# Kernel tuning notes

Hardware: AMD Instinct MI355X
Metric: run time of the kernel (lower is better)

## Reference

```python
import jax, jax.numpy as jnp
import numpy as np

CHANNELS = 256
NUM_HEADS = 4
NUM_GROUPS = 8
EPS = 1e-5


def setup_inputs() -> dict:
    key = jax.random.key(0)
    ks = jax.random.split(key, 7)
    c = CHANNELS
    x = jax.random.normal(ks[0], (2, c, 16, 16, 16), dtype=jnp.float32)
    # GroupNorm affine params (torch init: weight=1, bias=0)
    norm_w = jnp.ones((c,), dtype=jnp.float32)
    norm_b = jnp.zeros((c,), dtype=jnp.float32)
    # 1x1x1 Conv3d weights stored as [out_ch, in_ch]
    fan = 1.0 / np.sqrt(c)
    qkv_w = jax.random.uniform(ks[1], (3 * c, c), minval=-fan, maxval=fan, dtype=jnp.float32)
    qkv_b = jax.random.uniform(ks[2], (3 * c,), minval=-fan, maxval=fan, dtype=jnp.float32)
    proj_w = jax.random.uniform(ks[3], (c, c), minval=-fan, maxval=fan, dtype=jnp.float32)
    proj_b = jax.random.uniform(ks[4], (c,), minval=-fan, maxval=fan, dtype=jnp.float32)
    return {"x": x, "norm_w": norm_w, "norm_b": norm_b,
            "qkv_w": qkv_w, "qkv_b": qkv_b, "proj_w": proj_w, "proj_b": proj_b}


def _group_norm(x, w, b):
    B, C, D, H, W = x.shape
    g = NUM_GROUPS
    xg = x.reshape(B, g, C // g, D, H, W)
    mean = xg.mean(axis=(2, 3, 4, 5), keepdims=True)
    var = xg.var(axis=(2, 3, 4, 5), keepdims=True)
    xg = (xg - mean) * jax.lax.rsqrt(var + EPS)
    x = xg.reshape(B, C, D, H, W)
    return x * w[None, :, None, None, None] + b[None, :, None, None, None]


def _conv1x1(x, w, b):
    # x: [B, Cin, D, H, W], w: [Cout, Cin]
    y = jnp.einsum('bcdhw,oc->bodhw', x, w)
    return y + b[None, :, None, None, None]


def reference(x, norm_w, norm_b, qkv_w, qkv_b, proj_w, proj_b):
    B, C, D, H, W = x.shape
    N = D * H * W
    hd = C // NUM_HEADS
    x_norm = _group_norm(x, norm_w, norm_b)
    qkv = _conv1x1(x_norm, qkv_w, qkv_b)  # [B, 3C, D, H, W]
    q, k, v = jnp.split(qkv, 3, axis=1)
    q = q.reshape(B, NUM_HEADS, hd, N)
    k = k.reshape(B, NUM_HEADS, hd, N)
    v = v.reshape(B, NUM_HEADS, hd, N)
    scale = hd ** -0.5
    # attn[b,h,n,m] = softmax_m(q[:, :, :, n] . k[:, :, :, m] * scale)
    scores = jnp.einsum('bhcn,bhcm->bhnm', q, k) * scale
    attn = jax.nn.softmax(scores, axis=-1)
    out = jnp.einsum('bhcm,bhnm->bhcn', v, attn)
    out = out.reshape(B, C, D, H, W)
    return _conv1x1(out, proj_w, proj_b) + x
```

## Files before the change

kernel.cpp:

```cpp
#include <hip/hip_runtime.h>
#include <hip/hip_bf16.h>

#define NSP 4096
#define CH 256
#define NB 2
#define NG 8
#define CPG 32
#define NHD 4
#define HDIM 64

typedef unsigned short u16;
typedef unsigned int u32;
typedef __attribute__((ext_vector_type(8))) short bf16x8;
typedef __attribute__((ext_vector_type(4))) float f32x4;

#define MFMA __builtin_amdgcn_mfma_f32_16x16x32_bf16
#define QSCALE 0.18033688f

__device__ __forceinline__ u16 f2bf(float f) {
    u32 i = __float_as_uint(f);
    u32 r = (i + 0x7FFFu + ((i >> 16) & 1u)) >> 16;
    return (u16)r;
}

__device__ __forceinline__ void dma16(const u16* g, u16* l) {
    __builtin_amdgcn_global_load_lds(
        (const __attribute__((address_space(1))) void*)g,
        (__attribute__((address_space(3))) void*)l, 16, 0, 0);
}

__global__ __launch_bounds__(256) void prep(const float* __restrict__ qw,
                                            const float* __restrict__ pw,
                                            u16* __restrict__ wqb,
                                            u16* __restrict__ wpb,
                                            const float* __restrict__ x,
                                            float* __restrict__ partial) {
    if (blockIdx.x < 256) {
        int i = (blockIdx.x * 256 + threadIdx.x) * 4;
        const float* src; u16* dstbase; int j;
        if (i < 3 * CH * CH) { src = qw + i; dstbase = wqb; j = i; }
        else { j = i - 3 * CH * CH; src = pw + j; dstbase = wpb; }
        int m = j >> 8, c = j & 255;
        int dc = ((((c >> 3) ^ (m & 7)) << 3)) | (c & 7);
        float4 v = *(const float4*)src;
        ushort4 o;
        o.x = f2bf(v.x); o.y = f2bf(v.y); o.z = f2bf(v.z); o.w = f2bf(v.w);
        *(ushort4*)(dstbase + (m << 8) + dc) = o;
        return;
    }
    const int id = blockIdx.x - 256;
    const int bg = id >> 4, chunk = id & 15;
    const float* p = x + (size_t)bg * (CPG * NSP) + chunk * 8192;
    float s = 0.f, ss = 0.f;
    for (int i = threadIdx.x; i < 2048; i += 256) {
        float4 u = ((const float4*)p)[i];
        s += u.x + u.y + u.z + u.w;
        ss += u.x * u.x + u.y * u.y + u.z * u.z + u.w * u.w;
    }
    for (int off = 32; off > 0; off >>= 1) {
        s += __shfl_down(s, off);
        ss += __shfl_down(ss, off);
    }
    __shared__ float red[4][2];
    const int wv = threadIdx.x >> 6;
    if ((threadIdx.x & 63) == 0) { red[wv][0] = s; red[wv][1] = ss; }
    __syncthreads();
    if (threadIdx.x == 0) {
        float ts = red[0][0] + red[1][0] + red[2][0] + red[3][0];
        float tq = red[0][1] + red[1][1] + red[2][1] + red[3][1];
        partial[(bg * 16 + chunk) * 2]     = ts;
        partial[(bg * 16 + chunk) * 2 + 1] = tq;
    }
}

__global__ __launch_bounds__(256) void gn_apply_t(const float* __restrict__ x,
                                                  const float* __restrict__ partial,
                                                  const float* __restrict__ w,
                                                  const float* __restrict__ b,
                                                  u16* __restrict__ xnT) {
    __shared__ u16 T[64][72];
    const int n0 = blockIdx.x * 64, c0 = blockIdx.y * 64, bb = blockIdx.z;
    const int t = threadIdx.x;
    const int rc = t & 63;
    const int g  = t >> 6;
    const int c  = c0 + rc;
    const int bg = bb * NG + c / CPG;
    float s = 0.f, q = 0.f;
#pragma unroll
    for (int j = 0; j < 16; ++j) {
        s += partial[(bg * 16 + j) * 2];
        q += partial[(bg * 16 + j) * 2 + 1];
    }
    const float cnt = (float)(CPG * NSP);
    float mean = s / cnt;
    float var  = q / cnt - mean * mean;
    float rstd = rsqrtf(var + 1e-5f);
    float wf = w[c] * rstd, bv = b[c] - mean * wf;
    const float* px = x + ((size_t)bb * CH + c) * NSP + n0 + g * 16;
#pragma unroll
    for (int i = 0; i < 4; ++i) {
        float4 v = *(const float4*)(px + i * 4);
        T[g * 16 + i * 4 + 0][rc] = f2bf(v.x * wf + bv);
        T[g * 16 + i * 4 + 1][rc] = f2bf(v.y * wf + bv);
        T[g * 16 + i * 4 + 2][rc] = f2bf(v.z * wf + bv);
        T[g * 16 + i * 4 + 3][rc] = f2bf(v.w * wf + bv);
    }
    __syncthreads();
    int n = t >> 2, ch = (t & 3) * 16;
    uint4 o0 = *(const uint4*)&T[n][ch];
    uint4 o1 = *(const uint4*)&T[n][ch + 8];
    const int sw = n & 7;
    const int chunk0 = (c0 + ch) >> 3;
    u16* rowp = xnT + ((size_t)bb * NSP + n0 + n) * CH;
    *(uint4*)(rowp + ((chunk0 ^ sw) << 3))       = o0;
    *(uint4*)(rowp + (((chunk0 + 1) ^ sw) << 3)) = o1;
}

__global__ __launch_bounds__(256, 2) void gemm_qkv(const u16* __restrict__ Aw,
                                                   const float* __restrict__ bias,
                                                   const u16* __restrict__ xnT,
                                                   u16* __restrict__ qT,
                                                   u16* __restrict__ kT,
                                                   u16* __restrict__ v) {
    __shared__ u16 As[64][256];
    __shared__ u16 Bs[64][256];
    const int n0 = blockIdx.x * 64, m0 = blockIdx.y * 64, bb = blockIdx.z;
    const int wave = threadIdx.x >> 6, lane = threadIdx.x & 63;
    const int lq = lane & 15, quad = lane >> 4;
#pragma unroll
    for (int j = 0; j < 8; ++j) {
        int r2 = (wave * 8 + j) * 2;
        dma16(Aw + (size_t)(m0 + r2) * CH + lane * 8, &As[r2][0]);
        dma16(xnT + ((size_t)bb * NSP + n0 + r2) * CH + lane * 8, &Bs[r2][0]);
    }
    __syncthreads();
    const int wm = (wave >> 1) * 32, wn = (wave & 1) * 32;
    const int sw = lq & 7;
    f32x4 acc[2][2] = {};
#pragma unroll
    for (int kk = 0; kk < 8; ++kk) {
        bf16x8 a[2], b[2];
#pragma unroll
        for (int mt = 0; mt < 2; ++mt)
            a[mt] = *(const bf16x8*)&As[wm + mt * 16 + lq][(((kk * 4 + quad) ^ sw)) << 3];
#pragma unroll
        for (int nt = 0; nt < 2; ++nt)
            b[nt] = *(const bf16x8*)&Bs[wn + nt * 16 + lq][(((kk * 4 + quad) ^ sw)) << 3];
#pragma unroll
        for (int mt = 0; mt < 2; ++mt)
#pragma unroll
            for (int nt = 0; nt < 2; ++nt)
                acc[mt][nt] = MFMA(a[mt], b[nt], acc[mt][nt], 0, 0, 0);
    }
    const int sect = m0 >> 8;
    const int h = (m0 & 255) >> 6;
    const float osc = (sect == 0) ? QSCALE : 1.f;
#pragma unroll
    for (int im = 0; im < 2; ++im) {
        int ml = wm + im * 16 + quad * 4;
        float4 bs = *(const float4*)(bias + m0 + ml);
#pragma unroll
        for (int in = 0; in < 2; ++in) {
            int n = n0 + wn + in * 16 + lq;
            f32x4 a = acc[im][in];
            float v0 = (a[0] + bs.x) * osc, v1 = (a[1] + bs.y) * osc;
            float v2 = (a[2] + bs.z) * osc, v3 = (a[3] + bs.w) * osc;
            if (sect < 2) {
                int lc = ml >> 3, sub = ml & 7;
                int colp = ((lc ^ (n & 7)) << 3) | sub;
                u16* base = (sect ? kT : qT) +
                            (((size_t)bb * NHD + h) * NSP + n) * HDIM + colp;
                ushort4 o;
                o.x = f2bf(v0); o.y = f2bf(v1); o.z = f2bf(v2); o.w = f2bf(v3);
                *(ushort4*)base = o;
            } else {
                float vv[4] = {v0, v1, v2, v3};
#pragma unroll
                for (int r = 0; r < 4; ++r) {
                    int ch = (m0 - 512) + ml + r;
                    int pos = (n & ~63) + ((((n >> 3) & 7) ^ (ch & 7)) << 3) + (n & 7);
                    v[((size_t)bb * CH + ch) * NSP + pos] = f2bf(vv[r]);
                }
            }
        }
    }
}

__global__ __launch_bounds__(512, 2) void attn10(const u16* __restrict__ qT,
                                                 const u16* __restrict__ kT,
                                                 const u16* __restrict__ vN,
                                                 u16* __restrict__ aoT) {
    __shared__ u16 Ks[2][2][64][64];
    __shared__ u16 Vs[2][2][64][64];
    __shared__ __align__(16) char smem_ps[8 * 32 * 72 * 2];
    __shared__ float Ml[8][2][16];
    u16 (*Ps)[32][72] = reinterpret_cast<u16(*)[32][72]>(smem_ps);
    float (*Obuf)[32][68] = reinterpret_cast<float(*)[32][68]>(smem_ps);

    const int h = blockIdx.y, bb = blockIdx.z;
    const int t = threadIdx.x;
    const int wave = t >> 6, lane = t & 63;
    const int qg = wave & 3, kh = wave >> 2;
    const int lq = lane & 15, quad = lane >> 4;
    const int q_lo = blockIdx.x * 128 + qg * 32;

    const int pr = quad ^ (lq & 7);
    const u16* qrow0 = qT + (((size_t)bb * NHD + h) * NSP + q_lo + lq) * HDIM;
    bf16x8 qf[2][2];
    qf[0][0] = *(const bf16x8*)(qrow0 + pr * 8);
    qf[0][1] = *(const bf16x8*)(qrow0 + (pr ^ 4) * 8);
    qf[1][0] = *(const bf16x8*)(qrow0 + 16 * HDIM + pr * 8);
    qf[1][1] = *(const bf16x8*)(qrow0 + 16 * HDIM + (pr ^ 4) * 8);

    const u16* khead = kT + ((size_t)bb * NHD + h) * NSP * (size_t)HDIM;
    const u16* vhead = vN + ((size_t)bb * CH + h * HDIM) * NSP;

    const int sK   = (wave < 4);
    const int kh_s = (wave >> 1) & 1;
    const int rbase = (wave & 1) * 32;
    {
#pragma unroll
        for (int j = 0; j < 4; ++j) {
            int r8 = rbase + j * 8;
            if (sK) {
                dma16(khead + (size_t)(kh_s * 2048 + r8) * HDIM + lane * 8,
                      &Ks[kh_s][0][r8][0]);
            } else {
                dma16(vhead + (size_t)(r8 + (lane >> 3)) * NSP + kh_s * 2048 + (lane & 7) * 8,
                      &Vs[kh_s][0][r8][0]);
            }
        }
    }

    float l[2] = {0.f, 0.f};
    f32x4 O[2][4] = {};
    for (int kt = 0; kt < 32; ++kt) {
        const int cur = kt & 1;
        __syncthreads();
        if (kt < 31) {
            const int K1 = (kt + 1) * 64;
#pragma unroll
            for (int j = 0; j < 4; ++j) {
                int r8 = rbase + j * 8;
                if (sK) {
                    dma16(khead + (size_t)(kh_s * 2048 + K1 + r8) * HDIM + lane * 8,
                          &Ks[kh_s][cur ^ 1][r8][0]);
                } else {
                    dma16(vhead + (size_t)(r8 + (lane >> 3)) * NSP + kh_s * 2048 + K1 + (lane & 7) * 8,
                          &Vs[kh_s][cur ^ 1][r8][0]);
                }
            }
        }
        f32x4 st[2][4];
#pragma unroll
        for (int mt = 0; mt < 4; ++mt) {
            bf16x8 a0 = *(const bf16x8*)&Ks[kh][cur][mt * 16 + lq][pr * 8];
            bf16x8 a1 = *(const bf16x8*)&Ks[kh][cur][mt * 16 + lq][(pr ^ 4) * 8];
#pragma unroll
            for (int qt = 0; qt < 2; ++qt) {
                f32x4 acc = {0.f, 0.f, 0.f, 0.f};
                acc = MFMA(a0, qf[qt][0], acc, 0, 0, 0);
                acc = MFMA(a1, qf[qt][1], acc, 0, 0, 0);
                st[qt][mt] = acc;
            }
        }
#pragma unroll
        for (int qt = 0; qt < 2; ++qt) {
            float sum = 0.f;
#pragma unroll
            for (int mt = 0; mt < 4; ++mt) {
                float p0 = __builtin_amdgcn_exp2f(st[qt][mt][0]);
                float p1 = __builtin_amdgcn_exp2f(st[qt][mt][1]);
                float p2 = __builtin_amdgcn_exp2f(st[qt][mt][2]);
                float p3 = __builtin_amdgcn_exp2f(st[qt][mt][3]);
                sum += (p0 + p1) + (p2 + p3);
                u32 r0 = __float_as_uint(p0) + 0x8000u;
                u32 r1 = __float_as_uint(p1) + 0x8000u;
                u32 r2 = __float_as_uint(p2) + 0x8000u;
                u32 r3 = __float_as_uint(p3) + 0x8000u;
                uint2 pkk;
                pkk.x = __builtin_amdgcn_perm(r1, r0, 0x07060302);
                pkk.y = __builtin_amdgcn_perm(r3, r2, 0x07060302);
                *(uint2*)&Ps[wave][qt * 16 + lq][mt * 16 + quad * 4] = pkk;
            }
            l[qt] += sum;
        }
        bf16x8 pf[2][2];
        pf[0][0] = *(const bf16x8*)&Ps[wave][lq][quad * 8];
        pf[0][1] = *(const bf16x8*)&Ps[wave][lq][32 + quad * 8];
        pf[1][0] = *(const bf16x8*)&Ps[wave][16 + lq][quad * 8];
        pf[1][1] = *(const bf16x8*)&Ps[wave][16 + lq][32 + quad * 8];
#pragma unroll
        for (int mtc = 0; mtc < 4; ++mtc) {
            bf16x8 v0 = *(const bf16x8*)&Vs[kh][cur][mtc * 16 + lq][pr * 8];
            bf16x8 v1 = *(const bf16x8*)&Vs[kh][cur][mtc * 16 + lq][(pr ^ 4) * 8];
#pragma unroll
            for (int qt = 0; qt < 2; ++qt) {
                O[qt][mtc] = MFMA(v0, pf[qt][0], O[qt][mtc], 0, 0, 0);
                O[qt][mtc] = MFMA(v1, pf[qt][1], O[qt][mtc], 0, 0, 0);
            }
        }
    }
#pragma unroll
    for (int qt = 0; qt < 2; ++qt) {
        l[qt] += __shfl_xor(l[qt], 16);
        l[qt] += __shfl_xor(l[qt], 32);
    }
    if (lane < 16) { Ml[wave][0][lane] = l[0]; Ml[wave][1][lane] = l[1]; }
    __syncthreads();
    float gl[2];
    gl[0] = l[0] + Ml[wave ^ 4][0][lq];
    gl[1] = l[1] + Ml[wave ^ 4][1][lq];
    if (kh == 1) {
#pragma unroll
        for (int qt = 0; qt < 2; ++qt)
#pragma unroll
            for (int mtc = 0; mtc < 4; ++mtc)
                *(f32x4*)&Obuf[qg][qt * 16 + lq][mtc * 16 + quad * 4] = O[qt][mtc];
    }
    __syncthreads();
    if (kh == 0) {
        const int sw = lq & 7;
#pragma unroll
        for (int qt = 0; qt < 2; ++qt) {
            float linv = 1.f / gl[qt];
            u16* rowp = aoT + ((size_t)bb * NSP + q_lo + qt * 16 + lq) * CH;
#pragma unroll
            for (int mtc = 0; mtc < 4; ++mtc) {
                f32x4 sres = O[qt][mtc] +
                             *(const f32x4*)&Obuf[qg][qt * 16 + lq][mtc * 16 + quad * 4];
                ushort4 o;
                o.x = f2bf(sres[0] * linv);
                o.y = f2bf(sres[1] * linv);
                o.z = f2bf(sres[2] * linv);
                o.w = f2bf(sres[3] * linv);
                int chunk = (h << 3) | (mtc << 1) | (quad >> 1);
                int col = ((chunk ^ sw) << 3) | ((quad & 1) << 2);
                *(ushort4*)(rowp + col) = o;
            }
        }
    }
}

__global__ __launch_bounds__(256, 2) void gemm_proj(const u16* __restrict__ Aw,
                                                    const float* __restrict__ bias,
                                                    const u16* __restrict__ aoT,
                                                    const float* __restrict__ xres,
                                                    float* __restrict__ out) {
    __shared__ u16 As[64][256];
    __shared__ u16 Bs[64][256];
    const int n0 = blockIdx.x * 64, m0 = blockIdx.y * 64, bb = blockIdx.z;
    const int wave = threadIdx.x >> 6, lane = threadIdx.x & 63;
    const int lq = lane & 15, quad = lane >> 4;
#pragma unroll
    for (int j = 0; j < 8; ++j) {
        int r2 = (wave * 8 + j) * 2;
        dma16(Aw + (size_t)(m0 + r2) * CH + lane * 8, &As[r2][0]);
        dma16(aoT + ((size_t)bb * NSP + n0 + r2) * CH + lane * 8, &Bs[r2][0]);
    }
    __syncthreads();
    const int wm = (wave >> 1) * 32, wn = (wave & 1) * 32;
    const int sw = lq & 7;
    f32x4 acc[2][2] = {};
#pragma unroll
    for (int kk = 0; kk < 8; ++kk) {
        bf16x8 a[2], b[2];
#pragma unroll
        for (int mt = 0; mt < 2; ++mt)
            a[mt] = *(const bf16x8*)&As[wm + mt * 16 + lq][(((kk * 4 + quad) ^ sw)) << 3];
#pragma unroll
        for (int nt = 0; nt < 2; ++nt)
            b[nt] = *(const bf16x8*)&Bs[wn + nt * 16 + lq][(((kk * 4 + quad) ^ sw)) << 3];
#pragma unroll
        for (int mt = 0; mt < 2; ++mt)
#pragma unroll
            for (int nt = 0; nt < 2; ++nt)
                acc[mt][nt] = MFMA(a[mt], b[nt], acc[mt][nt], 0, 0, 0);
    }
#pragma unroll
    for (int im = 0; im < 2; ++im) {
        int ml = wm + im * 16 + quad * 4;
        float4 bs = *(const float4*)(bias + m0 + ml);
        float bsv[4] = {bs.x, bs.y, bs.z, bs.w};
#pragma unroll
        for (int in = 0; in < 2; ++in) {
            int n = n0 + wn + in * 16 + lq;
            f32x4 a = acc[im][in];
#pragma unroll
            for (int r = 0; r < 4; ++r) {
                size_t idx = ((size_t)bb * CH + m0 + ml + r) * NSP + n;
                out[idx] = a[r] + bsv[r] + xres[idx];
            }
        }
    }
}

extern "C" void kernel_launch(void* const* d_in, const int* in_sizes, int n_in,
                              void* d_out, int out_size, void* d_ws, size_t ws_size,
                              hipStream_t stream) {
    const float* x      = (const float*)d_in[0];
    const float* norm_w = (const float*)d_in[1];
    const float* norm_b = (const float*)d_in[2];
    const float* qkv_w  = (const float*)d_in[3];
    const float* qkv_b  = (const float*)d_in[4];
    const float* proj_w = (const float*)d_in[5];
    const float* proj_b = (const float*)d_in[6];
    float* out = (float*)d_out;

    char* w = (char*)d_ws;
    float* partial = (float*)w;
    u16* wqb = (u16*)(w + 4096);
    u16* wpb = (u16*)(w + 4096 + 393216);
    u16* xnT = (u16*)(w + 528384);
    u16* qT  = (u16*)(w + 528384 + 4194304);
    u16* kT  = (u16*)(w + 528384 + 2 * 4194304);
    u16* v   = (u16*)(w + 528384 + 3 * 4194304);
    u16* aoT = xnT;

    prep<<<dim3(512), 256, 0, stream>>>(qkv_w, proj_w, wqb, wpb, x, partial);
    gn_apply_t<<<dim3(NSP / 64, CH / 64, NB), 256, 0, stream>>>(
        x, partial, norm_w, norm_b, xnT);
    gemm_qkv<<<dim3(NSP / 64, (3 * CH) / 64, NB), 256, 0, stream>>>(
        wqb, qkv_b, xnT, qT, kT, v);
    attn10<<<dim3(NSP / 128, NHD, NB), 512, 0, stream>>>(qT, kT, v, aoT);
    gemm_proj<<<dim3(NSP / 64, CH / 64, NB), 256, 0, stream>>>(
        wpb, proj_b, aoT, x, out);
}
```

Baseline: 144.9 us.

## Halve attention query tile per block and swizzle the P buffer in LDS

```diff
diff --git a/kernel.cpp b/kernel.cpp
--- a/kernel.cpp
+++ b/kernel.cpp
@@ -186,31 +186,28 @@
     }
 }
 
-__global__ __launch_bounds__(512, 2) void attn10(const u16* __restrict__ qT,
+__global__ __launch_bounds__(512, 4) void attn11(const u16* __restrict__ qT,
                                                  const u16* __restrict__ kT,
                                                  const u16* __restrict__ vN,
                                                  u16* __restrict__ aoT) {
-    __shared__ u16 Ks[2][2][64][64];
-    __shared__ u16 Vs[2][2][64][64];
-    __shared__ __align__(16) char smem_ps[8 * 32 * 72 * 2];
-    __shared__ float Ml[8][2][16];
-    u16 (*Ps)[32][72] = reinterpret_cast<u16(*)[32][72]>(smem_ps);
-    float (*Obuf)[32][68] = reinterpret_cast<float(*)[32][68]>(smem_ps);
+    __shared__ __align__(16) char smem[81920];
+    u16 (*Ks)[2][64][64] = reinterpret_cast<u16(*)[2][64][64]>(smem);
+    u16 (*Vs)[2][64][64] = reinterpret_cast<u16(*)[2][64][64]>(smem + 32768);
+    u16* Ps = (u16*)(smem + 65536);
+    float* MlA = (float*)smem;
+    float* Obuf = (float*)(smem + 65536);
 
     const int h = blockIdx.y, bb = blockIdx.z;
     const int t = threadIdx.x;
     const int wave = t >> 6, lane = t & 63;
     const int qg = wave & 3, kh = wave >> 2;
     const int lq = lane & 15, quad = lane >> 4;
-    const int q_lo = blockIdx.x * 128 + qg * 32;
+    const int q_lo = blockIdx.x * 64 + qg * 16;
 
     const int pr = quad ^ (lq & 7);
     const u16* qrow0 = qT + (((size_t)bb * NHD + h) * NSP + q_lo + lq) * HDIM;
-    bf16x8 qf[2][2];
-    qf[0][0] = *(const bf16x8*)(qrow0 + pr * 8);
-    qf[0][1] = *(const bf16x8*)(qrow0 + (pr ^ 4) * 8);
-    qf[1][0] = *(const bf16x8*)(qrow0 + 16 * HDIM + pr * 8);
-    qf[1][1] = *(const bf16x8*)(qrow0 + 16 * HDIM + (pr ^ 4) * 8);
+    bf16x8 qf0 = *(const bf16x8*)(qrow0 + pr * 8);
+    bf16x8 qf1 = *(const bf16x8*)(qrow0 + (pr ^ 4) * 8);
 
     const u16* khead = kT + ((size_t)bb * NHD + h) * NSP * (size_t)HDIM;
     const u16* vhead = vN + ((size_t)bb * CH + h * HDIM) * NSP;
@@ -232,8 +229,11 @@
         }
     }
 
-    float l[2] = {0.f, 0.f};
-    f32x4 O[2][4] = {};
+    u16* psrow = Ps + (wave * 16 + lq) * 64;
+    const int sw2 = (lq & 7) << 1;
+
+    float l = 0.f;
+    f32x4 O[4] = {};
     for (int kt = 0; kt < 32; ++kt) {
         const int cur = kt & 1;
         __syncthreads();
@@ -251,93 +251,71 @@
                 }
             }
         }
-        f32x4 st[2][4];
+        f32x4 st[4];
 #pragma unroll
         for (int mt = 0; mt < 4; ++mt) {
             bf16x8 a0 = *(const bf16x8*)&Ks[kh][cur][mt * 16 + lq][pr * 8];
             bf16x8 a1 = *(const bf16x8*)&Ks[kh][cur][mt * 16 + lq][(pr ^ 4) * 8];
-#pragma unroll
-            for (int qt = 0; qt < 2; ++qt) {
-                f32x4 acc = {0.f, 0.f, 0.f, 0.f};
-                acc = MFMA(a0, qf[qt][0], acc, 0, 0, 0);
-                acc = MFMA(a1, qf[qt][1], acc, 0, 0, 0);
-                st[qt][mt] = acc;
-            }
-        }
-#pragma unroll
-        for (int qt = 0; qt < 2; ++qt) {
-            float sum = 0.f;
-#pragma unroll
-            for (int mt = 0; mt < 4; ++mt) {
-                float p0 = __builtin_amdgcn_exp2f(st[qt][mt][0]);
-                float p1 = __builtin_amdgcn_exp2f(st[qt][mt][1]);
-                float p2 = __builtin_amdgcn_exp2f(st[qt][mt][2]);
-                float p3 = __builtin_amdgcn_exp2f(st[qt][mt][3]);
-                sum += (p0 + p1) + (p2 + p3);
-                u32 r0 = __float_as_uint(p0) + 0x8000u;
-                u32 r1 = __float_as_uint(p1) + 0x8000u;
-                u32 r2 = __float_as_uint(p2) + 0x8000u;
-                u32 r3 = __float_as_uint(p3) + 0x8000u;
-                uint2 pkk;
-                pkk.x = __builtin_amdgcn_perm(r1, r0, 0x07060302);
-                pkk.y = __builtin_amdgcn_perm(r3, r2, 0x07060302);
-                *(uint2*)&Ps[wave][qt * 16 + lq][mt * 16 + quad * 4] = pkk;
-            }
-            l[qt] += sum;
-        }
-        bf16x8 pf[2][2];
-        pf[0][0] = *(const bf16x8*)&Ps[wave][lq][quad * 8];
-        pf[0][1] = *(const bf16x8*)&Ps[wave][lq][32 + quad * 8];
-        pf[1][0] = *(const bf16x8*)&Ps[wave][16 + lq][quad * 8];
-        pf[1][1] = *(const bf16x8*)&Ps[wave][16 + lq][32 + quad * 8];
+            f32x4 acc = {0.f, 0.f, 0.f, 0.f};
+            acc = MFMA(a0, qf0, acc, 0, 0, 0);
+            acc = MFMA(a1, qf1, acc, 0, 0, 0);
+            st[mt] = acc;
+        }
+        float sum = 0.f;
+#pragma unroll
+        for (int mt = 0; mt < 4; ++mt) {
+            float p0 = __builtin_amdgcn_exp2f(st[mt][0]);
+            float p1 = __builtin_amdgcn_exp2f(st[mt][1]);
+            float p2 = __builtin_amdgcn_exp2f(st[mt][2]);
+            float p3 = __builtin_amdgcn_exp2f(st[mt][3]);
+            sum += (p0 + p1) + (p2 + p3);
+            u32 r0 = __float_as_uint(p0) + 0x8000u;
+            u32 r1 = __float_as_uint(p1) + 0x8000u;
+            u32 r2 = __float_as_uint(p2) + 0x8000u;
+            u32 r3 = __float_as_uint(p3) + 0x8000u;
+            uint2 pkk;
+            pkk.x = __builtin_amdgcn_perm(r1, r0, 0x07060302);
+            pkk.y = __builtin_amdgcn_perm(r3, r2, 0x07060302);
+            *(uint2*)(psrow + (((mt * 4 + quad) ^ sw2) << 2)) = pkk;
+        }
+        l += sum;
+        bf16x8 pf0 = *(const bf16x8*)(psrow + ((((quad * 2)) ^ sw2) << 2));
+        bf16x8 pf1 = *(const bf16x8*)(psrow + (((8 + quad * 2) ^ sw2) << 2));
 #pragma unroll
         for (int mtc = 0; mtc < 4; ++mtc) {
             bf16x8 v0 = *(const bf16x8*)&Vs[kh][cur][mtc * 16 + lq][pr * 8];
             bf16x8 v1 = *(const bf16x8*)&Vs[kh][cur][mtc * 16 + lq][(pr ^ 4) * 8];
-#pragma unroll
-            for (int qt = 0; qt < 2; ++qt) {
-                O[qt][mtc] = MFMA(v0, pf[qt][0], O[qt][mtc], 0, 0, 0);
-                O[qt][mtc] = MFMA(v1, pf[qt][1], O[qt][mtc], 0, 0, 0);
-            }
-        }
-    }
-#pragma unroll
-    for (int qt = 0; qt < 2; ++qt) {
-        l[qt] += __shfl_xor(l[qt], 16);
-        l[qt] += __shfl_xor(l[qt], 32);
-    }
-    if (lane < 16) { Ml[wave][0][lane] = l[0]; Ml[wave][1][lane] = l[1]; }
-    __syncthreads();
-    float gl[2];
-    gl[0] = l[0] + Ml[wave ^ 4][0][lq];
-    gl[1] = l[1] + Ml[wave ^ 4][1][lq];
+            O[mtc] = MFMA(v0, pf0, O[mtc], 0, 0, 0);
+            O[mtc] = MFMA(v1, pf1, O[mtc], 0, 0, 0);
+        }
+    }
+    l += __shfl_xor(l, 16);
+    l += __shfl_xor(l, 32);
+    if (lane < 16) MlA[wave * 16 + lane] = l;
+    __syncthreads();
+    float gl = l + MlA[(wave ^ 4) * 16 + lq];
     if (kh == 1) {
 #pragma unroll
-        for (int qt = 0; qt < 2; ++qt)
-#pragma unroll
-            for (int mtc = 0; mtc < 4; ++mtc)
-                *(f32x4*)&Obuf[qg][qt * 16 + lq][mtc * 16 + quad * 4] = O[qt][mtc];
+        for (int mtc = 0; mtc < 4; ++mtc)
+            *(f32x4*)&Obuf[((size_t)qg * 16 + lq) * 64 + (((mtc * 4 + quad) ^ lq) << 2)] = O[mtc];
     }
     __syncthreads();
     if (kh == 0) {
         const int sw = lq & 7;
-#pragma unroll
-        for (int qt = 0; qt < 2; ++qt) {
-            float linv = 1.f / gl[qt];
-            u16* rowp = aoT + ((size_t)bb * NSP + q_lo + qt * 16 + lq) * CH;
-#pragma unroll
-            for (int mtc = 0; mtc < 4; ++mtc) {
-                f32x4 sres = O[qt][mtc] +
-                             *(const f32x4*)&Obuf[qg][qt * 16 + lq][mtc * 16 + quad * 4];
-                ushort4 o;
-                o.x = f2bf(sres[0] * linv);
-                o.y = f2bf(sres[1] * linv);
-                o.z = f2bf(sres[2] * linv);
-                o.w = f2bf(sres[3] * linv);
-                int chunk = (h << 3) | (mtc << 1) | (quad >> 1);
-                int col = ((chunk ^ sw) << 3) | ((quad & 1) << 2);
-                *(ushort4*)(rowp + col) = o;
-            }
+        float linv = 1.f / gl;
+        u16* rowp = aoT + ((size_t)bb * NSP + q_lo + lq) * CH;
+#pragma unroll
+        for (int mtc = 0; mtc < 4; ++mtc) {
+            f32x4 sres = O[mtc] +
+                         *(const f32x4*)&Obuf[((size_t)qg * 16 + lq) * 64 + (((mtc * 4 + quad) ^ lq) << 2)];
+            ushort4 o;
+            o.x = f2bf(sres[0] * linv);
+            o.y = f2bf(sres[1] * linv);
+            o.z = f2bf(sres[2] * linv);
+            o.w = f2bf(sres[3] * linv);
+            int chunk = (h << 3) | (mtc << 1) | (quad >> 1);
+            int col = ((chunk ^ sw) << 3) | ((quad & 1) << 2);
+            *(ushort4*)(rowp + col) = o;
         }
     }
 }
@@ -422,7 +400,7 @@
         x, partial, norm_w, norm_b, xnT);
     gemm_qkv<<<dim3(NSP / 64, (3 * CH) / 64, NB), 256, 0, stream>>>(
         wqb, qkv_b, xnT, qT, kT, v);
-    attn10<<<dim3(NSP / 128, NHD, NB), 512, 0, stream>>>(qT, kT, v, aoT);
+    attn11<<<dim3(NSP / 64, NHD, NB), 512, 0, stream>>>(qT, kT, v, aoT);
     gemm_proj<<<dim3(NSP / 64, CH / 64, NB), 256, 0, stream>>>(
         wpb, proj_b, aoT, x, out);
 }
```

Result: no change. 142.2 us (-1.9%).

## Rewrite attention with 32x32 MFMA, register P exchange, and 4-way key split

Applied to the files above, without the earlier changes.

```diff
diff --git a/kernel.cpp b/kernel.cpp
--- a/kernel.cpp
+++ b/kernel.cpp
@@ -13,8 +13,12 @@
 typedef unsigned int u32;
 typedef __attribute__((ext_vector_type(8))) short bf16x8;
 typedef __attribute__((ext_vector_type(4))) float f32x4;
+typedef __attribute__((ext_vector_type(16))) float f32x16;
+typedef __attribute__((ext_vector_type(2))) unsigned int u32x2;
+typedef __attribute__((ext_vector_type(4))) unsigned int u32x4;
 
 #define MFMA __builtin_amdgcn_mfma_f32_16x16x32_bf16
+#define MFMA32 __builtin_amdgcn_mfma_f32_32x32x16_bf16
 #define QSCALE 0.18033688f
 
 __device__ __forceinline__ u16 f2bf(float f) {
@@ -27,6 +31,20 @@
     __builtin_amdgcn_global_load_lds(
         (const __attribute__((address_space(1))) void*)g,
         (__attribute__((address_space(3))) void*)l, 16, 0, 0);
+}
+
+__device__ __forceinline__ void plswap(u32& a, u32& b) {
+#if __has_builtin(__builtin_amdgcn_permlane32_swap)
+    u32x2 r = __builtin_amdgcn_permlane32_swap(a, b, false, false);
+    a = r.x; b = r.y;
+#else
+    u32 sa = (u32)__shfl_xor((int)a, 32);
+    u32 sb = (u32)__shfl_xor((int)b, 32);
+    bool hi = (threadIdx.x & 32) != 0;
+    u32 na = hi ? sb : a;
+    u32 nb = hi ? b : sa;
+    a = na; b = nb;
+#endif
 }
 
 __global__ __launch_bounds__(256) void prep(const float* __restrict__ qw,
@@ -186,158 +204,208 @@
     }
 }
 
-__global__ __launch_bounds__(512, 2) void attn10(const u16* __restrict__ qT,
+__global__ __launch_bounds__(512, 2) void attn12(const u16* __restrict__ qT,
                                                  const u16* __restrict__ kT,
                                                  const u16* __restrict__ vN,
                                                  u16* __restrict__ aoT) {
-    __shared__ u16 Ks[2][2][64][64];
-    __shared__ u16 Vs[2][2][64][64];
-    __shared__ __align__(16) char smem_ps[8 * 32 * 72 * 2];
-    __shared__ float Ml[8][2][16];
-    u16 (*Ps)[32][72] = reinterpret_cast<u16(*)[32][72]>(smem_ps);
-    float (*Obuf)[32][68] = reinterpret_cast<float(*)[32][68]>(smem_ps);
+    __shared__ __align__(16) char smem[131072];
+    u16 (*Ks)[2][64][64] = reinterpret_cast<u16(*)[2][64][64]>(smem);
+    u16 (*Vs)[2][64][64] = reinterpret_cast<u16(*)[2][64][64]>(smem + 65536);
 
     const int h = blockIdx.y, bb = blockIdx.z;
     const int t = threadIdx.x;
     const int wave = t >> 6, lane = t & 63;
-    const int qg = wave & 3, kh = wave >> 2;
-    const int lq = lane & 15, quad = lane >> 4;
-    const int q_lo = blockIdx.x * 128 + qg * 32;
-
-    const int pr = quad ^ (lq & 7);
-    const u16* qrow0 = qT + (((size_t)bb * NHD + h) * NSP + q_lo + lq) * HDIM;
-    bf16x8 qf[2][2];
-    qf[0][0] = *(const bf16x8*)(qrow0 + pr * 8);
-    qf[0][1] = *(const bf16x8*)(qrow0 + (pr ^ 4) * 8);
-    qf[1][0] = *(const bf16x8*)(qrow0 + 16 * HDIM + pr * 8);
-    qf[1][1] = *(const bf16x8*)(qrow0 + 16 * HDIM + (pr ^ 4) * 8);
+    const int l31 = lane & 31, hi = lane >> 5, ln7 = lane & 7;
+    const int qg = wave >> 2;
+    const int csl = wave & 3;
+    const int q_lo = blockIdx.x * 128 + qg * 64;
+
+    bf16x8 qf[2][4];
+#pragma unroll
+    for (int qt = 0; qt < 2; ++qt) {
+        const u16* qrow = qT + (((size_t)bb * NHD + h) * NSP + q_lo + qt * 32 + l31) * HDIM;
+#pragma unroll
+        for (int d = 0; d < 4; ++d)
+            qf[qt][d] = *(const bf16x8*)(qrow + (((d * 2 + hi) ^ ln7) << 3));
+    }
 
     const u16* khead = kT + ((size_t)bb * NHD + h) * NSP * (size_t)HDIM;
     const u16* vhead = vN + ((size_t)bb * CH + h * HDIM) * NSP;
 
-    const int sK   = (wave < 4);
-    const int kh_s = (wave >> 1) & 1;
-    const int rbase = (wave & 1) * 32;
-    {
-#pragma unroll
-        for (int j = 0; j < 4; ++j) {
-            int r8 = rbase + j * 8;
-            if (sK) {
-                dma16(khead + (size_t)(kh_s * 2048 + r8) * HDIM + lane * 8,
-                      &Ks[kh_s][0][r8][0]);
-            } else {
-                dma16(vhead + (size_t)(r8 + (lane >> 3)) * NSP + kh_s * 2048 + (lane & 7) * 8,
-                      &Vs[kh_s][0][r8][0]);
-            }
-        }
+    const int sV  = wave >> 2;
+    const int ssl = wave & 3;
+    int koff[4];
+#pragma unroll
+    for (int d = 0; d < 4; ++d) koff[d] = (((d * 2 + hi) ^ ln7) << 3);
+
+#pragma unroll
+    for (int j = 0; j < 8; ++j) {
+        if (sV == 0)
+            dma16(khead + (size_t)(ssl * 1024 + j * 8) * HDIM + lane * 8,
+                  &Ks[ssl][0][j * 8][0]);
+        else
+            dma16(vhead + (size_t)(j * 8 + (lane >> 3)) * NSP + ssl * 1024 + (lane & 7) * 8,
+                  &Vs[ssl][0][j * 8][0]);
     }
 
     float l[2] = {0.f, 0.f};
-    f32x4 O[2][4] = {};
-    for (int kt = 0; kt < 32; ++kt) {
+    f32x16 O[2][2] = {};
+    for (int kt = 0; kt < 16; ++kt) {
         const int cur = kt & 1;
         __syncthreads();
-        if (kt < 31) {
+        if (kt < 15) {
             const int K1 = (kt + 1) * 64;
 #pragma unroll
-            for (int j = 0; j < 4; ++j) {
-                int r8 = rbase + j * 8;
-                if (sK) {
-                    dma16(khead + (size_t)(kh_s * 2048 + K1 + r8) * HDIM + lane * 8,
-                          &Ks[kh_s][cur ^ 1][r8][0]);
-                } else {
-                    dma16(vhead + (size_t)(r8 + (lane >> 3)) * NSP + kh_s * 2048 + K1 + (lane & 7) * 8,
-                          &Vs[kh_s][cur ^ 1][r8][0]);
-                }
-            }
-        }
-        f32x4 st[2][4];
-#pragma unroll
-        for (int mt = 0; mt < 4; ++mt) {
-            bf16x8 a0 = *(const bf16x8*)&Ks[kh][cur][mt * 16 + lq][pr * 8];
-            bf16x8 a1 = *(const bf16x8*)&Ks[kh][cur][mt * 16 + lq][(pr ^ 4) * 8];
+            for (int j = 0; j < 8; ++j) {
+                if (sV == 0)
+                    dma16(khead + (size_t)(ssl * 1024 + K1 + j * 8) * HDIM + lane * 8,
+                          &Ks[ssl][cur ^ 1][j * 8][0]);
+                else
+                    dma16(vhead + (size_t)(j * 8 + (lane >> 3)) * NSP + ssl * 1024 + K1 + (lane & 7) * 8,
+                          &Vs[ssl][cur ^ 1][j * 8][0]);
+            }
+        }
+#pragma unroll
+        for (int ktile = 0; ktile < 2; ++ktile) {
+            u32x4 pf[2][2];
 #pragma unroll
             for (int qt = 0; qt < 2; ++qt) {
-                f32x4 acc = {0.f, 0.f, 0.f, 0.f};
-                acc = MFMA(a0, qf[qt][0], acc, 0, 0, 0);
-                acc = MFMA(a1, qf[qt][1], acc, 0, 0, 0);
-                st[qt][mt] = acc;
-            }
-        }
+                f32x16 acc = {};
+#pragma unroll
+                for (int d = 0; d < 4; ++d) {
+                    bf16x8 kf = *(const bf16x8*)&Ks[csl][cur][ktile * 32 + l31][koff[d]];
+                    acc = MFMA32(kf, qf[qt][d], acc, 0, 0, 0);
+                }
+                float sum = 0.f;
+                u32 pk_[8];
+#pragma unroll
+                for (int g = 0; g < 4; ++g) {
+                    float p0 = __builtin_amdgcn_exp2f(acc[4 * g + 0]);
+                    float p1 = __builtin_amdgcn_exp2f(acc[4 * g + 1]);
+                    float p2 = __builtin_amdgcn_exp2f(acc[4 * g + 2]);
+                    float p3 = __builtin_amdgcn_exp2f(acc[4 * g + 3]);
+                    sum += (p0 + p1) + (p2 + p3);
+                    u32 r0 = __float_as_uint(p0) + 0x8000u;
+                    u32 r1 = __float_as_uint(p1) + 0x8000u;
+                    u32 r2 = __float_as_uint(p2) + 0x8000u;
+                    u32 r3 = __float_as_uint(p3) + 0x8000u;
+                    pk_[2 * g]     = __builtin_amdgcn_perm(r1, r0, 0x07060302);
+                    pk_[2 * g + 1] = __builtin_amdgcn_perm(r3, r2, 0x07060302);
+                }
+                l[qt] += sum;
+                plswap(pk_[0], pk_[2]); plswap(pk_[1], pk_[3]);
+                plswap(pk_[4], pk_[6]); plswap(pk_[5], pk_[7]);
+                pf[qt][0][0] = pk_[0]; pf[qt][0][1] = pk_[1];
+                pf[qt][0][2] = pk_[2]; pf[qt][0][3] = pk_[3];
+                pf[qt][1][0] = pk_[4]; pf[qt][1][1] = pk_[5];
+                pf[qt][1][2] = pk_[6]; pf[qt][1][3] = pk_[7];
+            }
+#pragma unroll
+            for (int ct = 0; ct < 2; ++ct)
+#pragma unroll
+                for (int s = 0; s < 2; ++s) {
+                    bf16x8 vf = *(const bf16x8*)
+                        &Vs[csl][cur][ct * 32 + l31][(((ktile * 4 + s * 2 + hi) ^ ln7) << 3)];
+                    bf16x8 pb0 = __builtin_bit_cast(bf16x8, pf[0][s]);
+                    bf16x8 pb1 = __builtin_bit_cast(bf16x8, pf[1][s]);
+                    O[0][ct] = MFMA32(vf, pb0, O[0][ct], 0, 0, 0);
+                    O[1][ct] = MFMA32(vf, pb1, O[1][ct], 0, 0, 0);
+                }
+        }
+    }
+    l[0] += __shfl_xor(l[0], 32);
+    l[1] += __shfl_xor(l[1], 32);
+    __syncthreads();
+    float* ob  = (float*)smem;
+    float* MlA = (float*)(smem + 65536);
+    if (lane < 32) {
+        MlA[(wave * 2 + 0) * 32 + l31] = l[0];
+        MlA[(wave * 2 + 1) * 32 + l31] = l[1];
+    }
+    if (csl >= 2) {
+        int slot = qg * 2 + (csl - 2);
+#pragma unroll
+        for (int qt = 0; qt < 2; ++qt)
+#pragma unroll
+            for (int ct = 0; ct < 2; ++ct) {
+                float* sp = ob + slot * 4096 + ((qt * 2 + ct) * 64 + lane) * 16;
+#pragma unroll
+                for (int cc = 0; cc < 4; ++cc) {
+                    f32x4 tmp = {O[qt][ct][4 * cc + 0], O[qt][ct][4 * cc + 1],
+                                 O[qt][ct][4 * cc + 2], O[qt][ct][4 * cc + 3]};
+                    *(f32x4*)(sp + ((cc ^ (lane & 3)) << 2)) = tmp;
+                }
+            }
+    }
+    __syncthreads();
+    if (csl < 2) {
+        int slot = qg * 2 + csl;
+#pragma unroll
+        for (int qt = 0; qt < 2; ++qt)
+#pragma unroll
+            for (int ct = 0; ct < 2; ++ct) {
+                float* sp = ob + slot * 4096 + ((qt * 2 + ct) * 64 + lane) * 16;
+#pragma unroll
+                for (int cc = 0; cc < 4; ++cc) {
+                    f32x4 tmp = *(const f32x4*)(sp + ((cc ^ (lane & 3)) << 2));
+                    O[qt][ct][4 * cc + 0] += tmp[0]; O[qt][ct][4 * cc + 1] += tmp[1];
+                    O[qt][ct][4 * cc + 2] += tmp[2]; O[qt][ct][4 * cc + 3] += tmp[3];
+                }
+            }
+    }
+    __syncthreads();
+    if (csl == 1) {
+#pragma unroll
+        for (int qt = 0; qt < 2; ++qt)
+#pragma unroll
+            for (int ct = 0; ct < 2; ++ct) {
+                float* sp = ob + qg * 4096 + ((qt * 2 + ct) * 64 + lane) * 16;
+#pragma unroll
+                for (int cc = 0; cc < 4; ++cc) {
+                    f32x4 tmp = {O[qt][ct][4 * cc + 0], O[qt][ct][4 * cc + 1],
+                                 O[qt][ct][4 * cc + 2], O[qt][ct][4 * cc + 3]};
+                    *(f32x4*)(sp + ((cc ^ (lane & 3)) << 2)) = tmp;
+                }
+            }
+    }
+    __syncthreads();
+    if (csl == 0) {
+#pragma unroll
+        for (int qt = 0; qt < 2; ++qt)
+#pragma unroll
+            for (int ct = 0; ct < 2; ++ct) {
+                float* sp = ob + qg * 4096 + ((qt * 2 + ct) * 64 + lane) * 16;
+#pragma unroll
+                for (int cc = 0; cc < 4; ++cc) {
+                    f32x4 tmp = *(const f32x4*)(sp + ((cc ^ (lane & 3)) << 2));
+                    O[qt][ct][4 * cc + 0] += tmp[0]; O[qt][ct][4 * cc + 1] += tmp[1];
+                    O[qt][ct][4 * cc + 2] += tmp[2]; O[qt][ct][4 * cc + 3] += tmp[3];
+                }
+            }
+        float gl[2], linv[2];
 #pragma unroll
         for (int qt = 0; qt < 2; ++qt) {
-            float sum = 0.f;
-#pragma unroll
-            for (int mt = 0; mt < 4; ++mt) {
-                float p0 = __builtin_amdgcn_exp2f(st[qt][mt][0]);
-                float p1 = __builtin_amdgcn_exp2f(st[qt][mt][1]);
-                float p2 = __builtin_amdgcn_exp2f(st[qt][mt][2]);
-                float p3 = __builtin_amdgcn_exp2f(st[qt][mt][3]);
-                sum += (p0 + p1) + (p2 + p3);
-                u32 r0 = __float_as_uint(p0) + 0x8000u;
-                u32 r1 = __float_as_uint(p1) + 0x8000u;
-                u32 r2 = __float_as_uint(p2) + 0x8000u;
-                u32 r3 = __float_as_uint(p3) + 0x8000u;
-                uint2 pkk;
-                pkk.x = __builtin_amdgcn_perm(r1, r0, 0x07060302);
-                pkk.y = __builtin_amdgcn_perm(r3, r2, 0x07060302);
-                *(uint2*)&Ps[wave][qt * 16 + lq][mt * 16 + quad * 4] = pkk;
-            }
-            l[qt] += sum;
-        }
-        bf16x8 pf[2][2];
-        pf[0][0] = *(const bf16x8*)&Ps[wave][lq][quad * 8];
-        pf[0][1] = *(const bf16x8*)&Ps[wave][lq][32 + quad * 8];
-        pf[1][0] = *(const bf16x8*)&Ps[wave][16 + lq][quad * 8];
-        pf[1][1] = *(const bf16x8*)&Ps[wave][16 + lq][32 + quad * 8];
-#pragma unroll
-        for (int mtc = 0; mtc < 4; ++mtc) {
-            bf16x8 v0 = *(const bf16x8*)&Vs[kh][cur][mtc * 16 + lq][pr * 8];
-            bf16x8 v1 = *(const bf16x8*)&Vs[kh][cur][mtc * 16 + lq][(pr ^ 4) * 8];
-#pragma unroll
-            for (int qt = 0; qt < 2; ++qt) {
-                O[qt][mtc] = MFMA(v0, pf[qt][0], O[qt][mtc], 0, 0, 0);
-                O[qt][mtc] = MFMA(v1, pf[qt][1], O[qt][mtc], 0, 0, 0);
-            }
-        }
-    }
-#pragma unroll
-    for (int qt = 0; qt < 2; ++qt) {
-        l[qt] += __shfl_xor(l[qt], 16);
-        l[qt] += __shfl_xor(l[qt], 32);
-    }
-    if (lane < 16) { Ml[wave][0][lane] = l[0]; Ml[wave][1][lane] = l[1]; }
-    __syncthreads();
-    float gl[2];
-    gl[0] = l[0] + Ml[wave ^ 4][0][lq];
-    gl[1] = l[1] + Ml[wave ^ 4][1][lq];
-    if (kh == 1) {
-#pragma unroll
-        for (int qt = 0; qt < 2; ++qt)
-#pragma unroll
-            for (int mtc = 0; mtc < 4; ++mtc)
-                *(f32x4*)&Obuf[qg][qt * 16 + lq][mtc * 16 + quad * 4] = O[qt][mtc];
-    }
-    __syncthreads();
-    if (kh == 0) {
-        const int sw = lq & 7;
+            gl[qt] = l[qt]
+                   + MlA[((qg * 4 + 1) * 2 + qt) * 32 + l31]
+                   + MlA[((qg * 4 + 2) * 2 + qt) * 32 + l31]
+                   + MlA[((qg * 4 + 3) * 2 + qt) * 32 + l31];
+            linv[qt] = 1.f / gl[qt];
+        }
 #pragma unroll
         for (int qt = 0; qt < 2; ++qt) {
-            float linv = 1.f / gl[qt];
-            u16* rowp = aoT + ((size_t)bb * NSP + q_lo + qt * 16 + lq) * CH;
-#pragma unroll
-            for (int mtc = 0; mtc < 4; ++mtc) {
-                f32x4 sres = O[qt][mtc] +
-                             *(const f32x4*)&Obuf[qg][qt * 16 + lq][mtc * 16 + quad * 4];
-                ushort4 o;
-                o.x = f2bf(sres[0] * linv);
-                o.y = f2bf(sres[1] * linv);
-                o.z = f2bf(sres[2] * linv);
-                o.w = f2bf(sres[3] * linv);
-                int chunk = (h << 3) | (mtc << 1) | (quad >> 1);
-                int col = ((chunk ^ sw) << 3) | ((quad & 1) << 2);
-                *(ushort4*)(rowp + col) = o;
-            }
+            u16* rowp = aoT + ((size_t)bb * NSP + q_lo + qt * 32 + l31) * CH;
+#pragma unroll
+            for (int ct = 0; ct < 2; ++ct)
+#pragma unroll
+                for (int g = 0; g < 4; ++g) {
+                    ushort4 o;
+                    o.x = f2bf(O[qt][ct][4 * g + 0] * linv[qt]);
+                    o.y = f2bf(O[qt][ct][4 * g + 1] * linv[qt]);
+                    o.z = f2bf(O[qt][ct][4 * g + 2] * linv[qt]);
+                    o.w = f2bf(O[qt][ct][4 * g + 3] * linv[qt]);
+                    int chunk = h * 8 + ct * 4 + g;
+                    *(ushort4*)(rowp + ((chunk ^ ln7) << 3) + (hi << 2)) = o;
+                }
         }
     }
 }
@@ -422,7 +490,7 @@
         x, partial, norm_w, norm_b, xnT);
     gemm_qkv<<<dim3(NSP / 64, (3 * CH) / 64, NB), 256, 0, stream>>>(
         wqb, qkv_b, xnT, qT, kT, v);
-    attn10<<<dim3(NSP / 128, NHD, NB), 512, 0, stream>>>(qT, kT, v, aoT);
+    attn12<<<dim3(NSP / 128, NHD, NB), 512, 0, stream>>>(qT, kT, v, aoT);
     gemm_proj<<<dim3(NSP / 64, CH / 64, NB), 256, 0, stream>>>(
         wpb, proj_b, aoT, x, out);
 }
```

New measurement: 133.0 us. -8.2%, faster.
